# Kernel tuning notes

Measured on AMD Instinct MI355X. Metric: run time of the kernel, lower is better.

## Reference

```python
import jax, jax.numpy as jnp
import numpy as np

N_NODES = 100000
N_EDGES = 1600000
NFEAT, NHID, NOUT = 128, 64, 32


def setup_inputs() -> dict:
    key = jax.random.key(0)
    ks = jax.random.split(key, 8)
    x = jax.random.normal(ks[0], (N_NODES, NFEAT), dtype=jnp.float32)
    adj_vals = jax.random.uniform(ks[1], (N_EDGES,), dtype=jnp.float32)
    W1 = jax.random.normal(ks[2], (NFEAT, NHID), dtype=jnp.float32) * (1.0 / np.sqrt(NFEAT))
    b1 = jnp.zeros((NHID,), dtype=jnp.float32)
    W2 = jax.random.normal(ks[3], (NHID, NOUT), dtype=jnp.float32) * (1.0 / np.sqrt(NHID))
    b2 = jnp.zeros((NOUT,), dtype=jnp.float32)
    edge_src = jax.random.randint(ks[4], (N_EDGES,), 0, N_NODES, dtype=jnp.int32)
    edge_dst = jax.random.randint(ks[5], (N_EDGES,), 0, N_NODES, dtype=jnp.int32)
    return {"x": x, "adj_vals": adj_vals, "W1": W1, "b1": b1, "W2": W2,
            "b2": b2, "edge_src": edge_src, "edge_dst": edge_dst}


def spmm(vals, src, dst, dense, n_nodes):
    # out[i, :] = sum_{e : dst[e]==i} vals[e] * dense[src[e], :]
    gathered = dense[src] * vals[:, None]          # [E, D] gather (memory-bound)
    return jax.ops.segment_sum(gathered, dst, num_segments=n_nodes)


def reference(x, adj_vals, W1, b1, W2, b2, edge_src, edge_dst):
    # GraphConvolution 1: support = x @ W1; out = adj @ support + b1; relu
    h = spmm(adj_vals, edge_src, edge_dst, x @ W1, N_NODES) + b1
    h = jax.nn.relu(h)
    # dropout is identity in eval mode (training=False)
    # GraphConvolution 2
    out = spmm(adj_vals, edge_src, edge_dst, h @ W2, N_NODES) + b2
    return out
```

## Files before the change

### kernel.cpp

```cpp
#include <hip/hip_runtime.h>
#include <hip/hip_fp16.h>

#define N_NODES 100000
#define N_EDGES 1600000
#define NFEAT 128
#define NHID 64
#define NOUT 32

#define NPB 256
#define NB ((N_NODES + NPB - 1) / NPB)
#define CAP 4608
#define CCH 2048
#define NCH ((N_EDGES + CCH - 1) / CCH)

typedef _Float16 half8 __attribute__((ext_vector_type(8)));
typedef float floatx4 __attribute__((ext_vector_type(4)));

__global__ __launch_bounds__(64) void wfrag_kernel(const float* __restrict__ W1,
                                                   __half* __restrict__ wfrag) {
    const int l  = threadIdx.x;
    const int b  = blockIdx.x;
    const int ks = b >> 2, ct = b & 3;
    const int kb = ks * 32 + (l >> 4) * 8;
    const int c  = ct * 16 + (l & 15);
    union { __half2 h2[4]; uint4 u; } pk;
#pragma unroll
    for (int j = 0; j < 4; ++j)
        pk.h2[j] = __floats2half2_rn(W1[(kb + 2 * j) * NHID + c],
                                     W1[(kb + 2 * j + 1) * NHID + c]);
    *(uint4*)&wfrag[((size_t)b * 64 + l) * 8] = pk.u;
}

__global__ __launch_bounds__(256) void gemm1_kernel(const float* __restrict__ x,
                                                    const __half* __restrict__ wfrag,
                                                    __half* __restrict__ support) {
    const int lane = threadIdx.x & 63;
    const int tile = blockIdx.x * 4 + (threadIdx.x >> 6);
    const int n0 = tile * 16;
    if (n0 >= N_NODES) return;

    half8 a[4][4];
#pragma unroll
    for (int ks = 0; ks < 4; ++ks)
#pragma unroll
        for (int ct = 0; ct < 4; ++ct)
            a[ks][ct] = *(const half8*)&wfrag[((size_t)(ks * 4 + ct) * 64 + lane) * 8];

    floatx4 acc[4];
#pragma unroll
    for (int ct = 0; ct < 4; ++ct) acc[ct] = (floatx4){0.f, 0.f, 0.f, 0.f};

    const int node = n0 + (lane & 15);
    const float* xrow = x + (size_t)node * NFEAT + (lane >> 4) * 8;

#pragma unroll
    for (int ks = 0; ks < 4; ++ks) {
        float4 f0 = *(const float4*)(xrow + ks * 32);
        float4 f1 = *(const float4*)(xrow + ks * 32 + 4);
        union { __half2 h2[4]; half8 v; } b;
        b.h2[0] = __floats2half2_rn(f0.x, f0.y);
        b.h2[1] = __floats2half2_rn(f0.z, f0.w);
        b.h2[2] = __floats2half2_rn(f1.x, f1.y);
        b.h2[3] = __floats2half2_rn(f1.z, f1.w);
#pragma unroll
        for (int ct = 0; ct < 4; ++ct)
            acc[ct] = __builtin_amdgcn_mfma_f32_16x16x32_f16(a[ks][ct], b.v, acc[ct], 0, 0, 0);
    }

    __half* srow = support + (size_t)node * NHID + (lane >> 4) * 4;
#pragma unroll
    for (int ct = 0; ct < 4; ++ct) {
        union { __half2 h2[2]; uint2 u; } pk;
        pk.h2[0] = __floats2half2_rn(acc[ct][0], acc[ct][1]);
        pk.h2[1] = __floats2half2_rn(acc[ct][2], acc[ct][3]);
        *(uint2*)&srow[ct * 16] = pk.u;
    }
}

__global__ __launch_bounds__(256) void init_gcur_kernel(int* __restrict__ gcur) {
    int i = blockIdx.x * 256 + threadIdx.x;
    if (i < NB) gcur[i] = i * CAP;
}

__global__ __launch_bounds__(256) void coarse_scatter_kernel(const float* __restrict__ vals,
                                                             const int* __restrict__ src,
                                                             const int* __restrict__ dst,
                                                             int* __restrict__ gcur,
                                                             uint2* __restrict__ recsC) {
    __shared__ int cnt[NB];
    __shared__ int sbase[NB];
    __shared__ int cur[NB];
    __shared__ int gbase[NB];
    __shared__ uint2 rl[CCH];
    __shared__ unsigned short slotB[CCH];
    __shared__ int scan_lds[256];
    const int tid = threadIdx.x;
    const int cbase0 = blockIdx.x * CCH;
    const int m = min(CCH, N_EDGES - cbase0);

    for (int i = tid; i < NB; i += 256) cnt[i] = 0;
    int dstv[CCH / 256];
    __syncthreads();
#pragma unroll
    for (int k = 0; k < CCH / 256; ++k) {
        int e = cbase0 + k * 256 + tid;
        int d = (e < N_EDGES) ? dst[e] : -1;
        dstv[k] = d;
        if (d >= 0) atomicAdd(&cnt[d >> 8], 1);
    }
    __syncthreads();
    {
        int v[4]; int tsum = 0;
#pragma unroll
        for (int i = 0; i < 4; ++i) {
            int idx = tid * 4 + i;
            v[i] = (idx < NB) ? cnt[idx] : 0;
            tsum += v[i];
        }
        scan_lds[tid] = tsum;
        __syncthreads();
        int val = tsum;
        for (int off = 1; off < 256; off <<= 1) {
            int add = (tid >= off) ? scan_lds[tid - off] : 0;
            __syncthreads();
            val += add;
            scan_lds[tid] = val;
            __syncthreads();
        }
        int excl = val - tsum;
#pragma unroll
        for (int i = 0; i < 4; ++i) {
            int idx = tid * 4 + i;
            if (idx < NB) { sbase[idx] = excl; cur[idx] = excl; excl += v[i]; }
        }
    }
    __syncthreads();
    for (int b = tid; b < NB; b += 256) {
        int c = cnt[b];
        gbase[b] = c ? atomicAdd(&gcur[b], c) : 0;
    }
#pragma unroll
    for (int k = 0; k < CCH / 256; ++k) {
        int e = cbase0 + k * 256 + tid;
        int d = dstv[k];
        if (d >= 0) {
            int b = d >> 8;
            int slot = atomicAdd(&cur[b], 1);
            rl[slot] = make_uint2((unsigned)src[e] | ((unsigned)(d & (NPB - 1)) << 17),
                                  __float_as_uint(vals[e]));
            slotB[slot] = (unsigned short)b;
        }
    }
    __syncthreads();
    for (int i = tid; i < m; i += 256) {
        int b = slotB[i];
        int idx = gbase[b] + (i - sbase[b]);
        if (idx < (b + 1) * CAP) recsC[idx] = rl[i];
    }
}

__global__ __launch_bounds__(256) void fine_sort_kernel(const int* __restrict__ gcur,
                                                        const uint2* __restrict__ recsC,
                                                        uint2* __restrict__ recs2,
                                                        int* __restrict__ offs,
                                                        int* __restrict__ ends) {
    __shared__ int cnt[NPB];
    __shared__ int cur[NPB];
    __shared__ int scan_lds[256];
    const int tid = threadIdx.x;
    const int b = blockIdx.x;
    const int s = b * CAP, e = gcur[b];
    cnt[tid] = 0;
    __syncthreads();
    for (int i = s + tid; i < e; i += 256)
        atomicAdd(&cnt[(recsC[i].x >> 17) & (NPB - 1)], 1);
    __syncthreads();
    int v = cnt[tid];
    scan_lds[tid] = v;
    __syncthreads();
    int val = v;
    for (int off = 1; off < 256; off <<= 1) {
        int add = (tid >= off) ? scan_lds[tid - off] : 0;
        __syncthreads();
        val += add;
        scan_lds[tid] = val;
        __syncthreads();
    }
    int excl = val - v;
    cur[tid] = excl;
    const int node = b * NPB + tid;
    if (node < N_NODES) {
        offs[node] = s + excl;
        ends[node] = s + excl + v;
    }
    __syncthreads();
    for (int i = s + tid; i < e; i += 256) {
        uint2 r = recsC[i];
        int dl = (r.x >> 17) & (NPB - 1);
        int p = atomicAdd(&cur[dl], 1);
        recs2[s + p] = make_uint2(r.x & 0x1FFFF, r.y);
    }
}

__global__ __launch_bounds__(256) void spmm1_kernel(const int* __restrict__ offs,
                                                    const int* __restrict__ ends,
                                                    const uint2* __restrict__ recs,
                                                    const __half* __restrict__ dense,
                                                    const float* __restrict__ b1,
                                                    __half* __restrict__ h) {
    __shared__ float red[4][8][65];
    const int tid = threadIdx.x;
    const int lane = tid & 63;
    const int wid = tid >> 6;
    const int d = blockIdx.x * 4 + wid;
    if (d >= N_NODES) return;
    const int g = lane >> 3, q = lane & 7;
    float acc[8];
#pragma unroll
    for (int j = 0; j < 8; ++j) acc[j] = 0.f;

    const int start = offs[d], end = ends[d];
    for (int e = start + g; e < end; e += 8) {
        uint2 r = recs[e];
        float v = __uint_as_float(r.y);
        union { uint4 u; __half2 h2[4]; } rw;
        rw.u = *(const uint4*)((const char*)dense + ((size_t)r.x << 7) + (q << 4));
#pragma unroll
        for (int j = 0; j < 4; ++j) {
            float2 f = __half22float2(rw.h2[j]);
            acc[2 * j]     += v * f.x;
            acc[2 * j + 1] += v * f.y;
        }
    }
#pragma unroll
    for (int j = 0; j < 8; ++j) red[wid][g][q * 8 + j] = acc[j];
    __builtin_amdgcn_wave_barrier();
    float s = 0.f;
#pragma unroll
    for (int gg = 0; gg < 8; ++gg) s += red[wid][gg][lane];
    float hv = fmaxf(s + b1[lane], 0.f);
    h[(size_t)d * NHID + lane] = __float2half(hv);
}

__global__ __launch_bounds__(256) void gemm2_kernel(const __half* __restrict__ h,
                                                    const float* __restrict__ W2,
                                                    __half* __restrict__ s2) {
    __shared__ float wlds[NHID * NOUT];
    const int tid = threadIdx.x;
    for (int i = tid; i < NHID * NOUT; i += 256) wlds[i] = W2[i];

    const int cg = (tid & 7) * 4;
    const int ng = tid >> 3;
    const int n0 = blockIdx.x * 128 + ng * 4;

    int nidx[4];
#pragma unroll
    for (int i = 0; i < 4; ++i) {
        int n = n0 + i;
        nidx[i] = (n < N_NODES) ? n : (N_NODES - 1);
    }
    __syncthreads();

    float acc[4][4];
#pragma unroll
    for (int i = 0; i < 4; ++i)
#pragma unroll
        for (int j = 0; j < 4; ++j) acc[i][j] = 0.f;

    for (int k0 = 0; k0 < NHID; k0 += 8) {
        float hx[4][8];
#pragma unroll
        for (int i = 0; i < 4; ++i) {
            union { float4 f4; __half2 h2[4]; } u;
            u.f4 = *(const float4*)&h[(size_t)nidx[i] * NHID + k0];
#pragma unroll
            for (int j = 0; j < 4; ++j) {
                float2 f = __half22float2(u.h2[j]);
                hx[i][j * 2]     = f.x;
                hx[i][j * 2 + 1] = f.y;
            }
        }
#pragma unroll
        for (int kk = 0; kk < 8; ++kk) {
            float4 w = *(const float4*)&wlds[(k0 + kk) * NOUT + cg];
#pragma unroll
            for (int i = 0; i < 4; ++i) {
                float xv = hx[i][kk];
                acc[i][0] += w.x * xv; acc[i][1] += w.y * xv;
                acc[i][2] += w.z * xv; acc[i][3] += w.w * xv;
            }
        }
    }
#pragma unroll
    for (int i = 0; i < 4; ++i) {
        int n = n0 + i;
        if (n < N_NODES) {
            union { __half2 h2[2]; uint2 u; } pk;
            pk.h2[0] = __floats2half2_rn(acc[i][0], acc[i][1]);
            pk.h2[1] = __floats2half2_rn(acc[i][2], acc[i][3]);
            *(uint2*)&s2[(size_t)n * NOUT + cg] = pk.u;
        }
    }
}

__global__ __launch_bounds__(256) void spmm2_kernel(const int* __restrict__ offs,
                                                    const int* __restrict__ ends,
                                                    const uint2* __restrict__ recs,
                                                    const __half* __restrict__ dense,
                                                    const float* __restrict__ b2,
                                                    float* __restrict__ out) {
    __shared__ float red[4][16][33];
    const int tid = threadIdx.x;
    const int lane = tid & 63;
    const int wid = tid >> 6;
    const int d = blockIdx.x * 4 + wid;
    if (d >= N_NODES) return;
    const int g = lane >> 2, q = lane & 3;
    float acc[8];
#pragma unroll
    for (int j = 0; j < 8; ++j) acc[j] = 0.f;

    const int start = offs[d], end = ends[d];
    for (int e = start + g; e < end; e += 16) {
        uint2 r = recs[e];
        float v = __uint_as_float(r.y);
        union { uint4 u; __half2 h2[4]; } rw;
        rw.u = *(const uint4*)((const char*)dense + ((size_t)r.x << 6) + (q << 4));
#pragma unroll
        for (int j = 0; j < 4; ++j) {
            float2 f = __half22float2(rw.h2[j]);
            acc[2 * j]     += v * f.x;
            acc[2 * j + 1] += v * f.y;
        }
    }
#pragma unroll
    for (int j = 0; j < 8; ++j) red[wid][g][q * 8 + j] = acc[j];
    __builtin_amdgcn_wave_barrier();
    const int f = lane & 31, hi = lane >> 5;
    float s = 0.f;
#pragma unroll
    for (int t = 0; t < 8; ++t) s += red[wid][hi * 8 + t][f];
    s += __shfl_xor(s, 32, 64);
    if (hi == 0) out[(size_t)d * NOUT + f] = s + b2[f];
}

extern "C" void kernel_launch(void* const* d_in, const int* in_sizes, int n_in,
                              void* d_out, int out_size, void* d_ws, size_t ws_size,
                              hipStream_t stream) {
    const float* x        = (const float*)d_in[0];
    const float* adj_vals = (const float*)d_in[1];
    const float* W1       = (const float*)d_in[2];
    const float* b1       = (const float*)d_in[3];
    const float* W2       = (const float*)d_in[4];
    const float* b2       = (const float*)d_in[5];
    const int*   esrc     = (const int*)d_in[6];
    const int*   edst     = (const int*)d_in[7];
    float*       out      = (float*)d_out;

    char* W = (char*)d_ws;
    __half* support = (__half*)W;
    __half* h       = (__half*)(W + 12800000);
    uint2*  recsC   = (uint2*)(W + 25600000);
    uint2*  recs2   = (uint2*)(W + 25600000 + (size_t)NB * CAP * 8);
    int*    IW      = (int*)(W + 25600000 + 2 * (size_t)NB * CAP * 8);
    int*    offs    = IW;
    int*    ends    = IW + 100032;
    int*    gcur    = IW + 200064;
    __half* wfrag   = (__half*)(IW + 200064 + 512);
    __half* s2      = support;

    wfrag_kernel<<<16, 64, 0, stream>>>(W1, wfrag);
    gemm1_kernel<<<(N_NODES / 16 + 3) / 4, 256, 0, stream>>>(x, wfrag, support);

    init_gcur_kernel<<<2, 256, 0, stream>>>(gcur);
    coarse_scatter_kernel<<<NCH, 256, 0, stream>>>(adj_vals, esrc, edst, gcur, recsC);
    fine_sort_kernel<<<NB, 256, 0, stream>>>(gcur, recsC, recs2, offs, ends);

    spmm1_kernel<<<(N_NODES + 3) / 4, 256, 0, stream>>>(offs, ends, recs2,
                                                        support, b1, h);

    gemm2_kernel<<<(N_NODES + 127) / 128, 256, 0, stream>>>(h, W2, s2);

    spmm2_kernel<<<(N_NODES + 3) / 4, 256, 0, stream>>>(offs, ends, recs2,
                                                        s2, b2, out);
}
```

Before: 159.9 us.

## Merge prep kernels and co-launch GEMM1 with coarse edge scatter

Folds the W1 fragment packing and gcur initialisation into one prep kernel, then runs the independent GEMM1 and coarse-scatter work as a single grid split by block index so the two overlap and fewer launches are issued. It also replaces the LDS Hillis-Steele block scan with a wave-shuffle scan that needs far fewer barriers, and clamps the fine-sort range to the bucket capacity. The cost is that GEMM1 blocks now reserve the scatter path's large shared-memory allocation, which may lower their occupancy.

```diff
diff --git a/kernel.cpp b/kernel.cpp
--- a/kernel.cpp
+++ b/kernel.cpp
@@ -12,150 +12,163 @@
 #define CAP 4608
 #define CCH 2048
 #define NCH ((N_EDGES + CCH - 1) / CCH)
+#define G1B ((N_NODES / 16 + 3) / 4)
 
 typedef _Float16 half8 __attribute__((ext_vector_type(8)));
 typedef float floatx4 __attribute__((ext_vector_type(4)));
 
-__global__ __launch_bounds__(64) void wfrag_kernel(const float* __restrict__ W1,
-                                                   __half* __restrict__ wfrag) {
-    const int l  = threadIdx.x;
-    const int b  = blockIdx.x;
-    const int ks = b >> 2, ct = b & 3;
-    const int kb = ks * 32 + (l >> 4) * 8;
-    const int c  = ct * 16 + (l & 15);
-    union { __half2 h2[4]; uint4 u; } pk;
-#pragma unroll
-    for (int j = 0; j < 4; ++j)
-        pk.h2[j] = __floats2half2_rn(W1[(kb + 2 * j) * NHID + c],
-                                     W1[(kb + 2 * j + 1) * NHID + c]);
-    *(uint4*)&wfrag[((size_t)b * 64 + l) * 8] = pk.u;
-}
-
-__global__ __launch_bounds__(256) void gemm1_kernel(const float* __restrict__ x,
-                                                    const __half* __restrict__ wfrag,
-                                                    __half* __restrict__ support) {
-    const int lane = threadIdx.x & 63;
-    const int tile = blockIdx.x * 4 + (threadIdx.x >> 6);
-    const int n0 = tile * 16;
-    if (n0 >= N_NODES) return;
-
-    half8 a[4][4];
-#pragma unroll
-    for (int ks = 0; ks < 4; ++ks)
-#pragma unroll
-        for (int ct = 0; ct < 4; ++ct)
-            a[ks][ct] = *(const half8*)&wfrag[((size_t)(ks * 4 + ct) * 64 + lane) * 8];
-
-    floatx4 acc[4];
-#pragma unroll
-    for (int ct = 0; ct < 4; ++ct) acc[ct] = (floatx4){0.f, 0.f, 0.f, 0.f};
-
-    const int node = n0 + (lane & 15);
-    const float* xrow = x + (size_t)node * NFEAT + (lane >> 4) * 8;
-
-#pragma unroll
-    for (int ks = 0; ks < 4; ++ks) {
-        float4 f0 = *(const float4*)(xrow + ks * 32);
-        float4 f1 = *(const float4*)(xrow + ks * 32 + 4);
-        union { __half2 h2[4]; half8 v; } b;
-        b.h2[0] = __floats2half2_rn(f0.x, f0.y);
-        b.h2[1] = __floats2half2_rn(f0.z, f0.w);
-        b.h2[2] = __floats2half2_rn(f1.x, f1.y);
-        b.h2[3] = __floats2half2_rn(f1.z, f1.w);
-#pragma unroll
-        for (int ct = 0; ct < 4; ++ct)
-            acc[ct] = __builtin_amdgcn_mfma_f32_16x16x32_f16(a[ks][ct], b.v, acc[ct], 0, 0, 0);
-    }
-
-    __half* srow = support + (size_t)node * NHID + (lane >> 4) * 4;
-#pragma unroll
-    for (int ct = 0; ct < 4; ++ct) {
-        union { __half2 h2[2]; uint2 u; } pk;
-        pk.h2[0] = __floats2half2_rn(acc[ct][0], acc[ct][1]);
-        pk.h2[1] = __floats2half2_rn(acc[ct][2], acc[ct][3]);
-        *(uint2*)&srow[ct * 16] = pk.u;
-    }
-}
-
-__global__ __launch_bounds__(256) void init_gcur_kernel(int* __restrict__ gcur) {
-    int i = blockIdx.x * 256 + threadIdx.x;
-    if (i < NB) gcur[i] = i * CAP;
-}
-
-__global__ __launch_bounds__(256) void coarse_scatter_kernel(const float* __restrict__ vals,
-                                                             const int* __restrict__ src,
-                                                             const int* __restrict__ dst,
-                                                             int* __restrict__ gcur,
-                                                             uint2* __restrict__ recsC) {
+__device__ __forceinline__ int wave_incl_scan(int v, int lane) {
+#pragma unroll
+    for (int d = 1; d < 64; d <<= 1) {
+        int t = __shfl_up(v, d, 64);
+        if (lane >= d) v += t;
+    }
+    return v;
+}
+__device__ __forceinline__ int block_excl_scan_256(int tsum, int tid, int* w4) {
+    const int lane = tid & 63, wid = tid >> 6;
+    int incl = wave_incl_scan(tsum, lane);
+    if (lane == 63) w4[wid] = incl;
+    __syncthreads();
+    int wbase = 0;
+    if (wid > 0) wbase += w4[0];
+    if (wid > 1) wbase += w4[1];
+    if (wid > 2) wbase += w4[2];
+    return wbase + incl - tsum;
+}
+
+__global__ __launch_bounds__(64) void prep_kernel(const float* __restrict__ W1,
+                                                  __half* __restrict__ wfrag,
+                                                  int* __restrict__ gcur) {
+    const int l = threadIdx.x;
+    const int b = blockIdx.x;
+    if (b < 16) {
+        const int ks = b >> 2, ct = b & 3;
+        const int kb = ks * 32 + (l >> 4) * 8;
+        const int c  = ct * 16 + (l & 15);
+        union { __half2 h2[4]; uint4 u; } pk;
+#pragma unroll
+        for (int j = 0; j < 4; ++j)
+            pk.h2[j] = __floats2half2_rn(W1[(kb + 2 * j) * NHID + c],
+                                         W1[(kb + 2 * j + 1) * NHID + c]);
+        *(uint4*)&wfrag[((size_t)b * 64 + l) * 8] = pk.u;
+    } else {
+        int i = (b - 16) * 64 + l;
+        if (i < NB) gcur[i] = i * CAP;
+    }
+}
+
+__global__ __launch_bounds__(256) void g1cs_kernel(const float* __restrict__ x,
+                                                   const __half* __restrict__ wfrag,
+                                                   __half* __restrict__ support,
+                                                   const float* __restrict__ vals,
+                                                   const int* __restrict__ src,
+                                                   const int* __restrict__ dst,
+                                                   int* __restrict__ gcur,
+                                                   uint2* __restrict__ recsC) {
     __shared__ int cnt[NB];
     __shared__ int sbase[NB];
     __shared__ int cur[NB];
     __shared__ int gbase[NB];
     __shared__ uint2 rl[CCH];
     __shared__ unsigned short slotB[CCH];
-    __shared__ int scan_lds[256];
-    const int tid = threadIdx.x;
-    const int cbase0 = blockIdx.x * CCH;
-    const int m = min(CCH, N_EDGES - cbase0);
-
-    for (int i = tid; i < NB; i += 256) cnt[i] = 0;
-    int dstv[CCH / 256];
-    __syncthreads();
-#pragma unroll
-    for (int k = 0; k < CCH / 256; ++k) {
-        int e = cbase0 + k * 256 + tid;
-        int d = (e < N_EDGES) ? dst[e] : -1;
-        dstv[k] = d;
-        if (d >= 0) atomicAdd(&cnt[d >> 8], 1);
-    }
-    __syncthreads();
-    {
-        int v[4]; int tsum = 0;
-#pragma unroll
-        for (int i = 0; i < 4; ++i) {
-            int idx = tid * 4 + i;
-            v[i] = (idx < NB) ? cnt[idx] : 0;
-            tsum += v[i];
-        }
-        scan_lds[tid] = tsum;
+    __shared__ int w4[4];
+    const int tid = threadIdx.x;
+
+    if (blockIdx.x < NCH) {
+        const int cbase0 = blockIdx.x * CCH;
+        const int m = min(CCH, N_EDGES - cbase0);
+        for (int i = tid; i < NB; i += 256) cnt[i] = 0;
+        int dstv[CCH / 256];
         __syncthreads();
-        int val = tsum;
-        for (int off = 1; off < 256; off <<= 1) {
-            int add = (tid >= off) ? scan_lds[tid - off] : 0;
-            __syncthreads();
-            val += add;
-            scan_lds[tid] = val;
-            __syncthreads();
-        }
-        int excl = val - tsum;
-#pragma unroll
-        for (int i = 0; i < 4; ++i) {
-            int idx = tid * 4 + i;
-            if (idx < NB) { sbase[idx] = excl; cur[idx] = excl; excl += v[i]; }
-        }
-    }
-    __syncthreads();
-    for (int b = tid; b < NB; b += 256) {
-        int c = cnt[b];
-        gbase[b] = c ? atomicAdd(&gcur[b], c) : 0;
-    }
-#pragma unroll
-    for (int k = 0; k < CCH / 256; ++k) {
-        int e = cbase0 + k * 256 + tid;
-        int d = dstv[k];
-        if (d >= 0) {
-            int b = d >> 8;
-            int slot = atomicAdd(&cur[b], 1);
-            rl[slot] = make_uint2((unsigned)src[e] | ((unsigned)(d & (NPB - 1)) << 17),
-                                  __float_as_uint(vals[e]));
-            slotB[slot] = (unsigned short)b;
-        }
-    }
-    __syncthreads();
-    for (int i = tid; i < m; i += 256) {
-        int b = slotB[i];
-        int idx = gbase[b] + (i - sbase[b]);
-        if (idx < (b + 1) * CAP) recsC[idx] = rl[i];
+#pragma unroll
+        for (int k = 0; k < CCH / 256; ++k) {
+            int e = cbase0 + k * 256 + tid;
+            int d = (e < N_EDGES) ? dst[e] : -1;
+            dstv[k] = d;
+            if (d >= 0) atomicAdd(&cnt[d >> 8], 1);
+        }
+        __syncthreads();
+        {
+            int v[4]; int tsum = 0;
+#pragma unroll
+            for (int i = 0; i < 4; ++i) {
+                int idx = tid * 4 + i;
+                v[i] = (idx < NB) ? cnt[idx] : 0;
+                tsum += v[i];
+            }
+            int excl = block_excl_scan_256(tsum, tid, w4);
+#pragma unroll
+            for (int i = 0; i < 4; ++i) {
+                int idx = tid * 4 + i;
+                if (idx < NB) { sbase[idx] = excl; cur[idx] = excl; excl += v[i]; }
+            }
+        }
+        __syncthreads();
+        for (int b = tid; b < NB; b += 256) {
+            int c = cnt[b];
+            gbase[b] = c ? atomicAdd(&gcur[b], c) : 0;
+        }
+#pragma unroll
+        for (int k = 0; k < CCH / 256; ++k) {
+            int e = cbase0 + k * 256 + tid;
+            int d = dstv[k];
+            if (d >= 0) {
+                int b = d >> 8;
+                int slot = atomicAdd(&cur[b], 1);
+                rl[slot] = make_uint2((unsigned)src[e] | ((unsigned)(d & (NPB - 1)) << 17),
+                                      __float_as_uint(vals[e]));
+                slotB[slot] = (unsigned short)b;
+            }
+        }
+        __syncthreads();
+        for (int i = tid; i < m; i += 256) {
+            int b = slotB[i];
+            int idx = gbase[b] + (i - sbase[b]);
+            if (idx < (b + 1) * CAP) recsC[idx] = rl[i];
+        }
+    } else {
+        const int lane = tid & 63;
+        const int tile = (blockIdx.x - NCH) * 4 + (tid >> 6);
+        const int n0 = tile * 16;
+        if (n0 >= N_NODES) return;
+
+        half8 a[4][4];
+#pragma unroll
+        for (int ks = 0; ks < 4; ++ks)
+#pragma unroll
+            for (int ct = 0; ct < 4; ++ct)
+                a[ks][ct] = *(const half8*)&wfrag[((size_t)(ks * 4 + ct) * 64 + lane) * 8];
+
+        floatx4 acc[4];
+#pragma unroll
+        for (int ct = 0; ct < 4; ++ct) acc[ct] = (floatx4){0.f, 0.f, 0.f, 0.f};
+
+        const int node = n0 + (lane & 15);
+        const float* xrow = x + (size_t)node * NFEAT + (lane >> 4) * 8;
+
+#pragma unroll
+        for (int ks = 0; ks < 4; ++ks) {
+            float4 f0 = *(const float4*)(xrow + ks * 32);
+            float4 f1 = *(const float4*)(xrow + ks * 32 + 4);
+            union { __half2 h2[4]; half8 v; } bv;
+            bv.h2[0] = __floats2half2_rn(f0.x, f0.y);
+            bv.h2[1] = __floats2half2_rn(f0.z, f0.w);
+            bv.h2[2] = __floats2half2_rn(f1.x, f1.y);
+            bv.h2[3] = __floats2half2_rn(f1.z, f1.w);
+#pragma unroll
+            for (int ct = 0; ct < 4; ++ct)
+                acc[ct] = __builtin_amdgcn_mfma_f32_16x16x32_f16(a[ks][ct], bv.v, acc[ct], 0, 0, 0);
+        }
+
+        __half* srow = support + (size_t)node * NHID + (lane >> 4) * 4;
+#pragma unroll
+        for (int ct = 0; ct < 4; ++ct) {
+            union { __half2 h2[2]; uint2 u; } pk;
+            pk.h2[0] = __floats2half2_rn(acc[ct][0], acc[ct][1]);
+            pk.h2[1] = __floats2half2_rn(acc[ct][2], acc[ct][3]);
+            *(uint2*)&srow[ct * 16] = pk.u;
+        }
     }
 }
 
@@ -166,27 +179,18 @@
                                                         int* __restrict__ ends) {
     __shared__ int cnt[NPB];
     __shared__ int cur[NPB];
-    __shared__ int scan_lds[256];
+    __shared__ int w4[4];
     const int tid = threadIdx.x;
     const int b = blockIdx.x;
-    const int s = b * CAP, e = gcur[b];
+    const int s = b * CAP;
+    const int e = min(gcur[b], s + CAP);
     cnt[tid] = 0;
     __syncthreads();
     for (int i = s + tid; i < e; i += 256)
         atomicAdd(&cnt[(recsC[i].x >> 17) & (NPB - 1)], 1);
     __syncthreads();
     int v = cnt[tid];
-    scan_lds[tid] = v;
-    __syncthreads();
-    int val = v;
-    for (int off = 1; off < 256; off <<= 1) {
-        int add = (tid >= off) ? scan_lds[tid - off] : 0;
-        __syncthreads();
-        val += add;
-        scan_lds[tid] = val;
-        __syncthreads();
-    }
-    int excl = val - v;
+    int excl = block_excl_scan_256(v, tid, w4);
     cur[tid] = excl;
     const int node = b * NPB + tid;
     if (node < N_NODES) {
@@ -369,11 +373,11 @@
     __half* wfrag   = (__half*)(IW + 200064 + 512);
     __half* s2      = support;
 
-    wfrag_kernel<<<16, 64, 0, stream>>>(W1, wfrag);
-    gemm1_kernel<<<(N_NODES / 16 + 3) / 4, 256, 0, stream>>>(x, wfrag, support);
-
-    init_gcur_kernel<<<2, 256, 0, stream>>>(gcur);
-    coarse_scatter_kernel<<<NCH, 256, 0, stream>>>(adj_vals, esrc, edst, gcur, recsC);
+    prep_kernel<<<16 + (NB + 63) / 64, 64, 0, stream>>>(W1, wfrag, gcur);
+
+    g1cs_kernel<<<NCH + G1B, 256, 0, stream>>>(x, wfrag, support,
+                                               adj_vals, esrc, edst, gcur, recsC);
+
     fine_sort_kernel<<<NB, 256, 0, stream>>>(gcur, recsC, recs2, offs, ends);
 
     spmm1_kernel<<<(N_NODES + 3) / 4, 256, 0, stream>>>(offs, ends, recs2,
```

After: 153.8 us. 1.04x faster.
